# Optimization experiments

Hardware: AMD Instinct MI355X
Metric: run time of the kernel (lower is better)

The kernel has to match this reference:

```python
import jax, jax.numpy as jnp
import numpy as np

F_DIM = 4096
HID = 256
COR = 32
N_FRAMES = 200
NB = 30
TS = 9  # 4 + 5 time_steps


def _gru(xg, hg, wx, wh, bx, bh):
    # torch.nn.GRU cell math, gates ordered (r, z, n)
    gx = xg @ wx + bx
    gh = hg @ wh + bh
    xr, xz, xn = jnp.split(gx, 3, axis=-1)
    hr, hz, hn = jnp.split(gh, 3, axis=-1)
    r = jax.nn.sigmoid(xr + hr)
    z = jax.nn.sigmoid(xz + hz)
    n = jnp.tanh(xn + r * hn)
    return (1.0 - z) * n + z * hg


def _sattn(h, mask):
    # parameter-free scaled dot-product attention across active tracks
    d = jnp.asarray(h.shape[-1], h.dtype)
    s = (h @ h.T) / jnp.sqrt(d)
    s = jnp.where(mask[None, :], s, -1e9)
    a = jax.nn.softmax(s, axis=-1)
    out = a @ h
    return jnp.where(mask[:, None], out, h)


def setup_inputs() -> dict:
    key = jax.random.key(0)
    ks = jax.random.split(key, 20)
    flow = jax.random.normal(ks[0], (1, N_FRAMES, NB + 1, F_DIM), jnp.float32)
    x = jax.random.normal(ks[1], (1, N_FRAMES, NB + 1, F_DIM), jnp.float32)
    # y: [track_id, x1,y1,x2,y2, label, conf, d0..d5] -> 13 channels
    track = jnp.broadcast_to(jnp.arange(1, NB + 1, dtype=jnp.float32)[None, None, :, None], (1, N_FRAMES, NB, 1))
    coords = jax.random.uniform(ks[2], (1, N_FRAMES, NB, 4), jnp.float32, 0.0, 1000.0)
    label = jnp.round(jax.random.uniform(ks[3], (1, N_FRAMES, NB, 1), jnp.float32))
    conf = jax.random.uniform(ks[4], (1, N_FRAMES, NB, 1), jnp.float32)
    dist = jax.random.normal(ks[5], (1, N_FRAMES, NB, 6), jnp.float32)
    y = jnp.concatenate([track, coords, label, conf, dist], axis=-1)
    toa = jnp.ones((1, 1), jnp.float32)
    s = 0.02
    p = lambda k, shp: s * jax.random.normal(k, shp, jnp.float32)
    return {
        "x": x, "y": y, "toa": toa, "flow": flow,
        "W_rgb": p(ks[6], (F_DIM, HID)), "b_rgb": jnp.zeros((HID,), jnp.float32),
        "W_bb": p(ks[7], (5, HID)), "b_bb": jnp.zeros((HID,), jnp.float32),
        "W_dd": p(ks[8], (6, HID)), "b_dd": jnp.zeros((HID,), jnp.float32),
        "W_proj": p(ks[9], (HID, COR)), "b_proj": jnp.zeros((COR,), jnp.float32),
        "Wx_c": p(ks[10], (COR, 3 * COR)), "Wh_c": p(ks[11], (COR, 3 * COR)),
        "bx_c": jnp.zeros((3 * COR,), jnp.float32), "bh_c": jnp.zeros((3 * COR,), jnp.float32),
        "Wx_g": p(ks[12], (2 * HID, 3 * HID)), "Wh_g": p(ks[13], (HID, 3 * HID)),
        "bx_g": jnp.zeros((3 * HID,), jnp.float32), "bh_g": jnp.zeros((3 * HID,), jnp.float32),
        "W_out": p(ks[14], (2 * HID + COR, 1)), "b_out": jnp.zeros((1,), jnp.float32),
        "W_pbox": p(ks[15], (2 * HID + COR, 4 * TS)), "b_pbox": jnp.zeros((4 * TS,), jnp.float32),
    }


def reference(x, y, toa, flow, W_rgb, b_rgb, W_bb, b_bb, W_dd, b_dd, W_proj, b_proj,
              Wx_c, Wh_c, bx_c, bh_c, Wx_g, Wh_g, bx_g, bh_g, W_out, b_out, W_pbox, b_pbox):
    T = x.shape[1] - TS
    norm = jnp.array([1920.0, 1200.0, 1920.0, 1200.0], y.dtype)
    nb = y[0, :, :, 1:5] / norm                      # (N, 30, 4) normalized boxes
    # future targets: 9 future frames of normalized boxes, flattened -> (T, 30, 36)
    fut = jnp.concatenate([nb[1 + i:1 + i + T] for i in range(TS)], axis=-1)
    flow_f = flow[0, :T]                             # (T, 31, F)
    yf = y[0, :T]                                    # (T, 30, 13)
    nbf = nb[:T]
    act = yf[..., 0] != 0                            # (T, 30) active-track mask

    def step(carry, inp):
        h, hc, bacc, oacc = carry
        ft, yt, nbt, futt, at = inp
        atf = at.astype(h.dtype)
        rgb = jax.nn.relu(ft @ W_rgb + b_rgb)        # (31, H)
        img = jnp.broadcast_to(rgb[0], (NB, rgb.shape[-1]))
        comb = jnp.concatenate([rgb[1:], img], axis=-1)            # (30, 2H)
        bfeat = jax.nn.relu(jnp.concatenate([nbt, yt[:, 6:7]], axis=-1) @ W_bb + b_bb)
        dfeat = jax.nn.relu(yt[:, 7:13] @ W_dd + b_dd)
        xc = dfeat @ W_proj + b_proj
        hc_n = _gru(xc, hc, Wx_c, Wh_c, bx_c, bh_c)  # CorGRU, output_cor = hidden
        h_n = _gru(comb, h, Wx_g, Wh_g, bx_g, bh_g)
        feat = jnp.concatenate([h_n, bfeat, hc_n], axis=-1)        # (30, 2H+32)
        logit = (feat @ W_out + b_out)[:, 0]
        pbox = feat @ W_pbox + b_pbox                # (30, 36)
        d = pbox - futt
        ad = jnp.abs(d)
        sl1 = jnp.mean(jnp.where(ad < 1.0, 0.5 * d * d, ad - 0.5), axis=-1)  # SmoothL1 per box
        bacc = bacc + jnp.sum(sl1 * atf)
        tgt = yt[:, 5]
        bce = jnp.maximum(logit, 0.0) - logit * tgt + jnp.log1p(jnp.exp(-jnp.abs(logit)))
        oacc = oacc + 0.05 * jnp.sum(bce * atf)
        h2 = jnp.where(at[:, None], h_n, h)
        hc2 = jnp.where(at[:, None], hc_n, hc)
        return (_sattn(h2, at), _sattn(hc2, at), bacc, oacc), None

    init = (jnp.zeros((NB, HID), flow.dtype), jnp.zeros((NB, COR), flow.dtype),
            jnp.zeros((), flow.dtype), jnp.zeros((), flow.dtype))
    (h, hc, bbox_l, obj_l), _ = jax.lax.scan(step, init, (flow_f, yf, nbf, fut, act))
    total = obj_l + bbox_l + 0.3 * bbox_l            # object + bbox + inter(0.3*bbox)
    return total
```

## Files before the change

kernel.cpp:

```cpp
#include <hip/hip_runtime.h>
#include <math.h>
#include <stdint.h>

#define T_STEPS 191
#define NB1 31
#define YS 13
#define NBLK 8

typedef short bf8 __attribute__((ext_vector_type(8)));
typedef float f16x __attribute__((ext_vector_type(16)));

#define MFMA32 __builtin_amdgcn_mfma_f32_32x32x16_bf16

__device__ __forceinline__ float sigmoid_(float x) { return 1.f / (1.f + expf(-x)); }

__device__ __forceinline__ unsigned bf16b(float x){
  unsigned u = __float_as_uint(x);
  return (u + 0x7fffu + ((u>>16)&1u)) >> 16;
}
__device__ __forceinline__ float bf16f(unsigned b){ return __uint_as_float(b<<16); }

__device__ __forceinline__ bf8 ldfrag(const unsigned short* p, int slot){
  uint4 u = *reinterpret_cast<const uint4*>(p + slot*8);
  return __builtin_bit_cast(bf8, u);
}
__device__ __forceinline__ bf8 ldg4(const unsigned* p){
  uint4 u = *reinterpret_cast<const uint4*>(p);
  return __builtin_bit_cast(bf8, u);
}
__device__ __forceinline__ bf8 gather8(const unsigned short* fr, int base){
  unsigned w0 = (unsigned)fr[base]    | ((unsigned)fr[base+8]<<16);
  unsigned w1 = (unsigned)fr[base+16] | ((unsigned)fr[base+24]<<16);
  unsigned w2 = (unsigned)fr[base+32] | ((unsigned)fr[base+40]<<16);
  unsigned w3 = (unsigned)fr[base+48] | ((unsigned)fr[base+56]<<16);
  uint4 u; u.x=w0; u.y=w1; u.z=w2; u.w=w3;
  return __builtin_bit_cast(bf8, u);
}
__device__ __forceinline__ f16x zf16(){
  f16x v;
#pragma unroll
  for (int q=0;q<16;++q) v[q]=0.f;
  return v;
}
__device__ __forceinline__ int aslot(int m, int k){
  return ((k>>4)*64 + m + ((k>>3)&1)*32)*8 + (k&7);
}

__device__ __forceinline__ void store_dw_mall_f(float* p, float v) {
    asm volatile("global_store_dword %0, %1, off sc0 sc1"
                 :: "v"((uintptr_t)p), "v"(v) : "memory");
}
__device__ __forceinline__ void store_dw_mall_u(unsigned* p, unsigned v) {
    asm volatile("global_store_dword %0, %1, off sc0 sc1"
                 :: "v"((uintptr_t)p), "v"(v) : "memory");
}
__device__ __forceinline__ void atomic_inc_mall(unsigned* p) {
    asm volatile("global_atomic_add %0, %1, off sc1"
                 :: "v"((uintptr_t)p), "v"(1u) : "memory");
}
__device__ __forceinline__ unsigned load_u32_mall(const unsigned* p) {
    unsigned v;
    asm volatile("global_load_dword %0, %1, off sc0 sc1\n\ts_waitcnt vmcnt(0)"
                 : "=v"(v) : "v"((uintptr_t)p) : "memory");
    return v;
}

template <bool GATHER, bool RELU>
__global__ __launch_bounds__(256) void gemm_tiled(
    const float* __restrict__ A, const float* __restrict__ B,
    const float* __restrict__ bias, float* __restrict__ C,
    int M, int N, int K)
{
    __shared__ float As[16][65];
    __shared__ float Bs[16][65];
    const int tid = threadIdx.x;
    const int tm = tid >> 4, tn = tid & 15;
    const int rowBase = blockIdx.y * 64;
    const int colBase = blockIdx.x * 64;
    float acc[4][4] = {};
    for (int kt = 0; kt < K; kt += 16) {
        #pragma unroll
        for (int l = 0; l < 4; ++l) {
            const int idx = tid + l * 256;
            const int kk = idx & 15, rr = idx >> 4;
            const int row = rowBase + rr;
            float v = 0.f;
            if (row < M) {
                if (GATHER) {
                    const int t = row / 30, i = row - t * 30;
                    const int k = kt + kk;
                    const int src = (k < 256) ? ((t * NB1 + i + 1) * 256 + k)
                                              : (t * NB1 * 256 + (k - 256));
                    v = A[src];
                } else {
                    v = A[(size_t)row * K + kt + kk];
                }
            }
            As[kk][rr] = v;
            const int nn = idx & 63, k2 = idx >> 6;
            Bs[k2][nn] = B[(size_t)(kt + k2) * N + colBase + nn];
        }
        __syncthreads();
        #pragma unroll
        for (int kk = 0; kk < 16; ++kk) {
            float a[4], b[4];
            #pragma unroll
            for (int i = 0; i < 4; ++i) a[i] = As[kk][tm * 4 + i];
            #pragma unroll
            for (int j = 0; j < 4; ++j) b[j] = Bs[kk][tn * 4 + j];
            #pragma unroll
            for (int i = 0; i < 4; ++i)
                #pragma unroll
                for (int j = 0; j < 4; ++j)
                    acc[i][j] = fmaf(a[i], b[j], acc[i][j]);
        }
        __syncthreads();
    }
    #pragma unroll
    for (int i = 0; i < 4; ++i) {
        const int row = rowBase + tm * 4 + i;
        if (row < M) {
            #pragma unroll
            for (int j = 0; j < 4; ++j) {
                const int col = colBase + tn * 4 + j;
                float v = acc[i][j] + bias[col];
                if (RELU) v = fmaxf(v, 0.f);
                C[(size_t)row * N + col] = v;
            }
        }
    }
}

__global__ __launch_bounds__(256) void prep_wg(const float* __restrict__ Whg,
                                               unsigned* __restrict__ wpg)
{
    const int idx = blockIdx.x * 256 + threadIdx.x;
    const int j  = idx & 3;
    const int l  = (idx >> 2) & 63;
    const int kb = (idx >> 8) & 15;
    const int nt = idx >> 12;
    const int g = nt / 3, gate = nt - g * 3;
    const int col = gate * 256 + g * 32 + (l & 31);
    const int k2 = kb * 8 + ((l >> 5) << 2) + j;
    const unsigned lo = bf16b(Whg[(size_t)(2 * k2) * 768 + col]);
    const unsigned hi = bf16b(Whg[(size_t)(2 * k2 + 1) * 768 + col]);
    wpg[idx] = lo | (hi << 16);
}

__global__ __launch_bounds__(256) void prep_hd(const float* __restrict__ Wpbox,
                                               const float* __restrict__ Wout,
                                               unsigned* __restrict__ hdh,
                                               unsigned* __restrict__ hdl)
{
    const int idx = blockIdx.x * 256 + threadIdx.x;
    if (idx >= 9216) return;
    const int j = idx & 3;
    const int l = (idx >> 2) & 63;
    const int kbnt = idx >> 8;
    const int kb = kbnt % 18, nt = kbnt / 18;
    const int d = nt * 32 + (l & 31);
    const int k0 = kb * 16 + ((l >> 5) << 3) + 2 * j;
    float v0 = 0.f, v1 = 0.f;
    if (d < 37) {
        const int r0 = (k0 < 256) ? k0 : 512 + (k0 - 256);
        const int r1 = (k0 + 1 < 256) ? (k0 + 1) : 512 + (k0 + 1 - 256);
        v0 = (d < 36) ? Wpbox[(size_t)r0 * 36 + d] : Wout[r0];
        v1 = (d < 36) ? Wpbox[(size_t)r1 * 36 + d] : Wout[r1];
    }
    const unsigned h0 = bf16b(v0), h1 = bf16b(v1);
    const unsigned l0 = bf16b(v0 - bf16f(h0)), l1 = bf16b(v1 - bf16f(h1));
    hdh[idx] = h0 | (h1 << 16);
    hdl[idx] = l0 | (l1 << 16);
}

__global__ __launch_bounds__(256) void prep_hcw(const float* __restrict__ Whc,
                                                unsigned* __restrict__ hch,
                                                unsigned* __restrict__ hcl)
{
    const int idx = blockIdx.x * 256 + threadIdx.x;
    if (idx >= 1536) return;
    const int j = idx & 3;
    const int l = (idx >> 2) & 63;
    const int kb = (idx >> 8) & 1;
    const int nt = idx >> 9;
    const int col = nt * 32 + (l & 31);
    const int k0 = kb * 16 + ((l >> 5) << 3) + 2 * j;
    const float v0 = Whc[k0 * 96 + col];
    const float v1 = Whc[(k0 + 1) * 96 + col];
    const unsigned h0 = bf16b(v0), h1 = bf16b(v1);
    const unsigned l0 = bf16b(v0 - bf16f(h0)), l1 = bf16b(v1 - bf16f(h1));
    hch[idx] = h0 | (h1 << 16);
    hcl[idx] = l0 | (l1 << 16);
}

__global__ void prep_bias(const float* __restrict__ bxg, const float* __restrict__ bhg,
                          const float* __restrict__ bxc, const float* __restrict__ bhc,
                          float* __restrict__ biasg, float* __restrict__ biasc)
{
    const int t = threadIdx.x;
    if (t < 768) biasg[t] = bxg[t] + (t < 512 ? bhg[t] : 0.f);
    if (t < 96)  biasc[t] = bxc[t] + (t < 64 ? bhc[t] : 0.f);
}

__global__ __launch_bounds__(256) void precomp_kernel(
    const float* __restrict__ y,
    const float* __restrict__ Wbb, const float* __restrict__ bbb,
    const float* __restrict__ Wdd, const float* __restrict__ bdd,
    const float* __restrict__ Wproj, const float* __restrict__ bproj,
    const float* __restrict__ Wxc, const float* __restrict__ biasc,
    const float* __restrict__ Wpbox, const float* __restrict__ bpbox,
    const float* __restrict__ Wout, const float* __restrict__ bout,
    float* __restrict__ gxc, float* __restrict__ pbox_b, float* __restrict__ logit_b)
{
    const int m = blockIdx.x;
    const int tid = threadIdx.x;
    __shared__ float bf[256], df[256], xcs[32], yl[16];
    if (tid < YS) yl[tid] = y[m * YS + tid];
    __syncthreads();
    const float invnorm[4] = {1.f/1920.f, 1.f/1200.f, 1.f/1920.f, 1.f/1200.f};
    {
        float s = bbb[tid];
        s = fmaf(yl[1] * invnorm[0], Wbb[0 * 256 + tid], s);
        s = fmaf(yl[2] * invnorm[1], Wbb[1 * 256 + tid], s);
        s = fmaf(yl[3] * invnorm[2], Wbb[2 * 256 + tid], s);
        s = fmaf(yl[4] * invnorm[3], Wbb[3 * 256 + tid], s);
        s = fmaf(yl[6],              Wbb[4 * 256 + tid], s);
        bf[tid] = fmaxf(s, 0.f);
    }
    {
        float s = bdd[tid];
        #pragma unroll
        for (int k = 0; k < 6; ++k) s = fmaf(yl[7 + k], Wdd[k * 256 + tid], s);
        df[tid] = fmaxf(s, 0.f);
    }
    __syncthreads();
    {
        const int c = tid >> 3, p = tid & 7;
        float s = 0.f;
        for (int k = p; k < 256; k += 8) s = fmaf(df[k], Wproj[k * 32 + c], s);
        s += __shfl_xor(s, 1); s += __shfl_xor(s, 2); s += __shfl_xor(s, 4);
        if (p == 0) xcs[c] = s + bproj[c];
    }
    __syncthreads();
    if (tid < 96) {
        float s = biasc[tid];
        #pragma unroll
        for (int k = 0; k < 32; ++k) s = fmaf(xcs[k], Wxc[k * 96 + tid], s);
        gxc[m * 96 + tid] = s;
    }
    {
        const int d = tid >> 2, p = tid & 3;
        if (d < 37) {
            float s = 0.f;
            if (d < 36) {
                for (int k = p; k < 256; k += 4) s = fmaf(bf[k], Wpbox[(256 + k) * 36 + d], s);
            } else {
                for (int k = p; k < 256; k += 4) s = fmaf(bf[k], Wout[256 + k], s);
            }
            s += __shfl_xor(s, 1); s += __shfl_xor(s, 2);
            if (p == 0) {
                if (d < 36) pbox_b[m * 36 + d] = s + bpbox[d];
                else        logit_b[m] = s + bout[0];
            }
        }
    }
}

__global__ __launch_bounds__(512, 2) void seq8(
    const float* __restrict__ y,
    const float* __restrict__ gxg,
    const float* __restrict__ gxc,
    const float* __restrict__ pbox_b,
    const float* __restrict__ logit_b,
    const unsigned* __restrict__ wpg,
    const unsigned* __restrict__ hdh, const unsigned* __restrict__ hdl,
    const unsigned* __restrict__ hch, const unsigned* __restrict__ hcl,
    const float* __restrict__ bhg,
    const float* __restrict__ bhc,
    unsigned* __restrict__ h2x,
    float* __restrict__ pbx,
    unsigned* __restrict__ bar,
    float* __restrict__ parts)
{
    const int tid = threadIdx.x;
    const int bb = blockIdx.x;
    const int lane = tid & 63, wid = tid >> 6;
    const int half = lane >> 5, ln31 = lane & 31;

    __shared__ __align__(16) unsigned wgl[12288];
    __shared__ __align__(16) unsigned short hA_hi[8192], hA_lo[8192];
    __shared__ __align__(16) unsigned short hnf_hi[1024], hnf_lo[1024];
    __shared__ __align__(16) unsigned short cf_hi[1024],  cf_lo[1024];
    __shared__ __align__(16) unsigned short cnf_hi[1024], cnf_lo[1024];
    __shared__ __align__(16) unsigned short wf_hi[1024],  wf_lo[1024];
    __shared__ __align__(16) unsigned short cwf_hi[1024], cwf_lo[1024];
    __shared__ float exch[6144];
    __shared__ float gxgs[2880];
    __shared__ float gxcs[2880];
    __shared__ float hcst[1056];
    __shared__ float actf[32], bhnl[32], bhcl[32], red[16];

    {
        const unsigned* wsrc = wpg + (size_t)(3 * bb) * 4096;
        for (int i = tid; i < 12288; i += 512) wgl[i] = wsrc[i];
    }
    for (int i = tid; i < 8192; i += 512){ hA_hi[i] = 0; hA_lo[i] = 0; }
    for (int i = tid; i < 1024; i += 512){
        hnf_hi[i]=0; hnf_lo[i]=0; cf_hi[i]=0; cf_lo[i]=0;
        cnf_hi[i]=0; cnf_lo[i]=0; wf_hi[i]=0; wf_lo[i]=0;
        cwf_hi[i]=0; cwf_lo[i]=0;
    }
    for (int i = tid; i < 1056; i += 512) hcst[i] = 0.f;
    if (tid < 32){ bhnl[tid] = bhg[512 + bb*32 + tid]; bhcl[tid] = bhc[64 + tid]; }
    float bacc = 0.f, oacc = 0.f;
    __syncthreads();

    for (int t = 0; t < T_STEPS; ++t) {
        const int m0 = t * 30;
        const int dbuf = t & 1;
        unsigned* h2b = h2x + dbuf * 8192;
        float* pbb = pbx + dbuf * 9600;

        float4 sg0, sg1, sc0v, sc1v;
        const bool hasg = (tid < 360);
        if (hasg){
            { const int i = tid;       const int obj = i/24, r24 = i - obj*24;
              sg0 = *(const float4*)(gxg + (size_t)(m0+obj)*768 + (r24>>3)*256 + bb*32 + (r24&7)*4); }
            { const int i = tid + 360; const int obj = i/24, r24 = i - obj*24;
              sg1 = *(const float4*)(gxg + (size_t)(m0+obj)*768 + (r24>>3)*256 + bb*32 + (r24&7)*4); }
        }
        const bool hasc = (bb == 7) && (tid < 360);
        if (hasc){
            { const int i = tid;       const int obj = i/24, c4 = i - obj*24;
              sc0v = *(const float4*)(gxc + (size_t)(m0+obj)*96 + c4*4); }
            { const int i = tid + 360; const int obj = i/24, c4 = i - obj*24;
              sc1v = *(const float4*)(gxc + (size_t)(m0+obj)*96 + c4*4); }
        }
        if (tid < 32) actf[tid] = (tid < 30 && y[(size_t)(m0+tid)*YS] != 0.f) ? 1.f : 0.f;

        if (wid < 3){
            f16x acc = zf16();
            const unsigned* wb = wgl + wid * 4096;
#pragma unroll 4
            for (int kb = 0; kb < 16; ++kb){
                const bf8 bw = ldg4(wb + (kb*64 + lane)*4);
                const bf8 ah = ldfrag(hA_hi, kb*64 + lane);
                const bf8 al = ldfrag(hA_lo, kb*64 + lane);
                acc = MFMA32(ah, bw, acc, 0,0,0);
                acc = MFMA32(al, bw, acc, 0,0,0);
            }
#pragma unroll
            for (int q = 0; q < 16; ++q){
                const int row = (q&3) + ((q>>2)<<3) + (half<<2);
                exch[wid*1024 + row*32 + ln31] = acc[q];
            }
        } else if (wid < 6 && bb == 7){
            const int g3 = wid - 3;
            f16x acc = zf16();
#pragma unroll
            for (int kb = 0; kb < 2; ++kb){
                const bf8 ah = ldfrag(cf_hi, kb*64 + lane);
                const bf8 al = ldfrag(cf_lo, kb*64 + lane);
                const bf8 wh = ldg4(hch + ((g3*2 + kb)*64 + lane)*4);
                const bf8 wl = ldg4(hcl + ((g3*2 + kb)*64 + lane)*4);
                acc = MFMA32(ah, wh, acc, 0,0,0);
                acc = MFMA32(ah, wl, acc, 0,0,0);
                acc = MFMA32(al, wh, acc, 0,0,0);
            }
#pragma unroll
            for (int q = 0; q < 16; ++q){
                const int row = (q&3) + ((q>>2)<<3) + (half<<2);
                exch[(3+g3)*1024 + row*32 + ln31] = acc[q];
            }
        }
        if (hasg){
            { const int i = tid;       const int obj = i/24, r24 = i - obj*24;
              *(float4*)(gxgs + obj*96 + r24*4) = sg0; }
            { const int i = tid + 360; const int obj = i/24, r24 = i - obj*24;
              *(float4*)(gxgs + obj*96 + r24*4) = sg1; }
        }
        if (hasc){
            { const int i = tid;       const int obj = i/24, c4 = i - obj*24;
              *(float4*)(gxcs + obj*96 + c4*4) = sc0v; }
            { const int i = tid + 360; const int obj = i/24, c4 = i - obj*24;
              *(float4*)(gxcs + obj*96 + c4*4) = sc1v; }
        }
        __syncthreads();

        if (tid < 480){
#pragma unroll
            for (int s = 0; s < 2; ++s){
                const int e = tid*2 + s;
                const int obj = e >> 5, dim = e & 31;
                const float rv = sigmoid_(exch[obj*32 + dim]        + gxgs[obj*96 + dim]);
                const float zv = sigmoid_(exch[1024 + obj*32 + dim] + gxgs[obj*96 + 32 + dim]);
                const float nv = tanhf(gxgs[obj*96 + 64 + dim]
                                       + rv*(exch[2048 + obj*32 + dim] + bhnl[dim]));
                const int sl = aslot(obj, bb*32 + dim);
                const float h = bf16f(hA_hi[sl]) + bf16f(hA_lo[sl]);
                const float hnv = (1.f - zv)*nv + zv*h;
                const float h2 = (actf[obj] > 0.f) ? hnv : h;
                const unsigned hb = bf16b(h2), lb = bf16b(h2 - bf16f(hb));
                store_dw_mall_u(h2b + sl, hb | (lb << 16));
                const int sl2 = aslot(obj, dim);
                const unsigned nh = bf16b(hnv), nl = bf16b(hnv - bf16f(nh));
                hnf_hi[sl2] = (unsigned short)nh; hnf_lo[sl2] = (unsigned short)nl;
            }
            if (bb == 7){
#pragma unroll
                for (int s = 0; s < 2; ++s){
                    const int e = tid*2 + s;
                    const int obj = e >> 5, cd = e & 31;
                    const float rv = sigmoid_(exch[3072 + obj*32 + cd] + gxcs[obj*96 + cd]);
                    const float zv = sigmoid_(exch[4096 + obj*32 + cd] + gxcs[obj*96 + 32 + cd]);
                    const float nv = tanhf(gxcs[obj*96 + 64 + cd]
                                           + rv*(exch[5120 + obj*32 + cd] + bhcl[cd]));
                    const float hc = hcst[obj*33 + cd];
                    const float cnv = (1.f - zv)*nv + zv*hc;
                    const float c2 = (actf[obj] > 0.f) ? cnv : hc;
                    hcst[obj*33 + cd] = c2;
                    const int sl2 = aslot(obj, cd);
                    const unsigned hb = bf16b(c2), lb = bf16b(c2 - bf16f(hb));
                    cf_hi[sl2] = (unsigned short)hb; cf_lo[sl2] = (unsigned short)lb;
                    const unsigned nh = bf16b(cnv), nl = bf16b(cnv - bf16f(nh));
                    cnf_hi[sl2] = (unsigned short)nh; cnf_lo[sl2] = (unsigned short)nl;
                }
            }
        }
        __syncthreads();

        if (wid < 2){
            f16x hp = zf16();
#pragma unroll
            for (int kb = 0; kb < 2; ++kb){
                const bf8 ah = ldfrag(hnf_hi, kb*64 + lane);
                const bf8 al = ldfrag(hnf_lo, kb*64 + lane);
                const int kbg = 2*bb + kb;
                const bf8 wh = ldg4(hdh + ((wid*18 + kbg)*64 + lane)*4);
                const bf8 wl = ldg4(hdl + ((wid*18 + kbg)*64 + lane)*4);
                hp = MFMA32(ah, wh, hp, 0,0,0);
                hp = MFMA32(al, wh, hp, 0,0,0);
                hp = MFMA32(ah, wl, hp, 0,0,0);
            }
            if (bb == 7){
#pragma unroll
                for (int kb = 0; kb < 2; ++kb){
                    const bf8 ah = ldfrag(cnf_hi, kb*64 + lane);
                    const bf8 al = ldfrag(cnf_lo, kb*64 + lane);
                    const bf8 wh = ldg4(hdh + ((wid*18 + 16 + kb)*64 + lane)*4);
                    const bf8 wl = ldg4(hdl + ((wid*18 + 16 + kb)*64 + lane)*4);
                    hp = MFMA32(ah, wh, hp, 0,0,0);
                    hp = MFMA32(al, wh, hp, 0,0,0);
                    hp = MFMA32(ah, wl, hp, 0,0,0);
                }
            }
            const int d = wid*32 + ln31;
            if (d < 37){
#pragma unroll
                for (int q = 0; q < 16; ++q){
                    const int obj = (q&3) + ((q>>2)<<3) + (half<<2);
                    if (obj < 30) store_dw_mall_f(pbb + (obj*40 + d)*8 + bb, hp[q]);
                }
            }
        }

        asm volatile("s_waitcnt vmcnt(0)" ::: "memory");
        __syncthreads();
        if (tid == 0){
            atomic_inc_mall(bar);
            const unsigned tgtc = (unsigned)(NBLK * (t + 1));
            unsigned cur;
            do { asm volatile("s_sleep 1" :::); cur = load_u32_mall(bar); } while (cur < tgtc);
        }
        __syncthreads();

        {
            const int nOb = (bb == 7) ? 2 : 4;
            if (tid < nOb * 37){
                const int oo = tid / 37, d = tid - oo*37;
                const int obj = bb*4 + oo;
                if (actf[obj] > 0.f){
                    const float* pp = pbb + (obj*40 + d)*8;
                    float4 f0, f1;
                    asm volatile("global_load_dwordx4 %0, %2, off sc0 sc1\n\t"
                                 "global_load_dwordx4 %1, %3, off sc0 sc1\n\t"
                                 "s_waitcnt vmcnt(0)"
                                 : "=v"(f0), "=v"(f1)
                                 : "v"((uintptr_t)pp), "v"((uintptr_t)(pp+4)) : "memory");
                    const float sum8 = f0.x+f0.y+f0.z+f0.w + f1.x+f1.y+f1.z+f1.w;
                    const int m = m0 + obj;
                    if (d < 36){
                        const int s4 = d >> 2, cc = d & 3;
                        const float fn = (cc & 1) ? (1.f/1200.f) : (1.f/1920.f);
                        const float fu = y[(size_t)((t+1+s4)*30 + obj)*YS + 1 + cc] * fn;
                        const float df = sum8 + pbox_b[(size_t)m*36 + d] - fu;
                        const float ad = fabsf(df);
                        bacc += ((ad < 1.f) ? 0.5f*df*df : ad - 0.5f) * (1.f/36.f);
                    } else {
                        const float l = sum8 + logit_b[m];
                        const float tg = y[(size_t)m*YS + 5];
                        oacc += 0.05f * (fmaxf(l, 0.f) - l*tg + log1pf(expf(-fabsf(l))));
                    }
                }
            }
        }
        {
            unsigned uu[16];
#pragma unroll
            for (int j = 0; j < 16; ++j){
                const unsigned* sp = h2b + tid + j*512;
                asm volatile("global_load_dword %0, %1, off sc0 sc1"
                             : "=v"(uu[j]) : "v"((uintptr_t)sp) : "memory");
            }
            asm volatile("s_waitcnt vmcnt(0)" ::: "memory");
#pragma unroll
            for (int j = 0; j < 16; ++j){
                const int idx = tid + j*512;
                hA_hi[idx] = (unsigned short)(uu[j] & 0xffffu);
                hA_lo[idx] = (unsigned short)(uu[j] >> 16);
            }
        }
        __syncthreads();

        if (wid < 3){
            f16x s = zf16();
#pragma unroll 4
            for (int kb = 0; kb < 16; ++kb){
                const bf8 ah = ldfrag(hA_hi, kb*64 + lane);
                const bf8 al = ldfrag(hA_lo, kb*64 + lane);
                if (wid == 0)      s = MFMA32(ah, ah, s, 0,0,0);
                else if (wid == 1) s = MFMA32(ah, al, s, 0,0,0);
                else               s = MFMA32(al, ah, s, 0,0,0);
            }
#pragma unroll
            for (int q = 0; q < 16; ++q){
                const int row = (q&3) + ((q>>2)<<3) + (half<<2);
                exch[wid*1024 + row*32 + ln31] = s[q];
            }
        } else if (wid == 3 && bb == 7){
            f16x s = zf16();
#pragma unroll
            for (int kb = 0; kb < 2; ++kb){
                const bf8 ah = ldfrag(cf_hi, kb*64 + lane);
                const bf8 al = ldfrag(cf_lo, kb*64 + lane);
                s = MFMA32(ah, ah, s, 0,0,0);
                s = MFMA32(ah, al, s, 0,0,0);
                s = MFMA32(al, ah, s, 0,0,0);
            }
#pragma unroll
            for (int q = 0; q < 16; ++q){
                const int row = (q&3) + ((q>>2)<<3) + (half<<2);
                exch[3072 + row*32 + ln31] = s[q];
            }
        }
        __syncthreads();

        if (wid == 0 && lane < 30){
            float sv[30]; float mx = -1e30f;
#pragma unroll
            for (int j = 0; j < 30; ++j){
                float x = exch[lane*32 + j] + exch[1024 + lane*32 + j] + exch[2048 + lane*32 + j];
                x = (actf[j] > 0.f) ? x * 0.0625f : -1e9f;
                sv[j] = x; mx = fmaxf(mx, x);
            }
            float sum = 0.f;
#pragma unroll
            for (int j = 0; j < 30; ++j){ sv[j] = expf(sv[j] - mx); sum += sv[j]; }
            const float inv = 1.f / sum;
#pragma unroll
            for (int j = 0; j < 32; ++j){
                const float w = (j < 30) ? sv[j]*inv : 0.f;
                const unsigned hb = bf16b(w), lb = bf16b(w - bf16f(hb));
                const int sl = aslot(lane, j);
                wf_hi[sl] = (unsigned short)hb; wf_lo[sl] = (unsigned short)lb;
            }
        } else if (wid == 1 && bb == 7 && lane < 30){
            float sv[30]; float mx = -1e30f;
#pragma unroll
            for (int j = 0; j < 30; ++j){
                float x = exch[3072 + lane*32 + j];
                x = (actf[j] > 0.f) ? x * 0.17677669529663687f : -1e9f;
                sv[j] = x; mx = fmaxf(mx, x);
            }
            float sum = 0.f;
#pragma unroll
            for (int j = 0; j < 30; ++j){ sv[j] = expf(sv[j] - mx); sum += sv[j]; }
            const float inv = 1.f / sum;
#pragma unroll
            for (int j = 0; j < 32; ++j){
                const float w = (j < 30) ? sv[j]*inv : 0.f;
                const unsigned hb = bf16b(w), lb = bf16b(w - bf16f(hb));
                const int sl = aslot(lane, j);
                cwf_hi[sl] = (unsigned short)hb; cwf_lo[sl] = (unsigned short)lb;
            }
        }
        __syncthreads();

        {
            const int dd = wid*32 + ln31;
            f16x ao = zf16();
#pragma unroll
            for (int kb2 = 0; kb2 < 2; ++kb2){
                const bf8 wh = ldfrag(wf_hi, kb2*64 + lane);
                const bf8 wl = ldfrag(wf_lo, kb2*64 + lane);
                const int base = ((dd>>4)*64 + kb2*16 + (half<<3) + ((dd>>3)&1)*32)*8 + (dd&7);
                const bf8 bh = gather8(hA_hi, base);
                const bf8 bl = gather8(hA_lo, base);
                ao = MFMA32(wh, bh, ao, 0,0,0);
                ao = MFMA32(wh, bl, ao, 0,0,0);
                ao = MFMA32(wl, bh, ao, 0,0,0);
            }
#pragma unroll
            for (int q = 0; q < 16; ++q){
                const int obj = (q&3) + ((q>>2)<<3) + (half<<2);
                const int sl = aslot(obj, dd);
                const float h2v = bf16f(hA_hi[sl]) + bf16f(hA_lo[sl]);
                const float v = (actf[obj] > 0.f) ? ao[q] : h2v;
                const unsigned hb = bf16b(v), lb = bf16b(v - bf16f(hb));
                hA_hi[sl] = (unsigned short)hb; hA_lo[sl] = (unsigned short)lb;
            }
        }
        if (bb == 7 && wid == 0){
            f16x co = zf16();
#pragma unroll
            for (int kb2 = 0; kb2 < 2; ++kb2){
                const bf8 wh = ldfrag(cwf_hi, kb2*64 + lane);
                const bf8 wl = ldfrag(cwf_lo, kb2*64 + lane);
                const int base = ((ln31>>4)*64 + kb2*16 + (half<<3) + ((ln31>>3)&1)*32)*8 + (ln31&7);
                const bf8 bh = gather8(cf_hi, base);
                const bf8 bl = gather8(cf_lo, base);
                co = MFMA32(wh, bh, co, 0,0,0);
                co = MFMA32(wh, bl, co, 0,0,0);
                co = MFMA32(wl, bh, co, 0,0,0);
            }
#pragma unroll
            for (int q = 0; q < 16; ++q){
                const int obj = (q&3) + ((q>>2)<<3) + (half<<2);
                const float c2v = hcst[obj*33 + ln31];
                const float v = (actf[obj] > 0.f) ? co[q] : c2v;
                hcst[obj*33 + ln31] = v;
                const int sl = aslot(obj, ln31);
                const unsigned hb = bf16b(v), lb = bf16b(v - bf16f(hb));
                cf_hi[sl] = (unsigned short)hb; cf_lo[sl] = (unsigned short)lb;
            }
        }
        __syncthreads();
    }

#pragma unroll
    for (int o = 1; o < 64; o <<= 1){ bacc += __shfl_xor(bacc, o); oacc += __shfl_xor(oacc, o); }
    if (lane == 0){ red[wid] = bacc; red[8 + wid] = oacc; }
    __syncthreads();
    if (tid == 0){
        float b = 0.f, o = 0.f;
        for (int i = 0; i < 8; ++i){ b += red[i]; o += red[8 + i]; }
        parts[bb] = b; parts[8 + bb] = o;
    }
}

__global__ void reduce_kernel(const float* __restrict__ parts, float* __restrict__ out) {
    if (threadIdx.x == 0) {
        float b = 0.f, o = 0.f;
        for (int i = 0; i < NBLK; ++i) { b += parts[i]; o += parts[8 + i]; }
        out[0] = o + 1.3f * b;
    }
}

extern "C" void kernel_launch(void* const* d_in, const int* in_sizes, int n_in,
                              void* d_out, int out_size, void* d_ws, size_t ws_size,
                              hipStream_t stream) {
    (void)in_sizes; (void)n_in; (void)out_size; (void)ws_size;
    const float* y      = (const float*)d_in[1];
    const float* flow   = (const float*)d_in[3];
    const float* W_rgb  = (const float*)d_in[4];
    const float* b_rgb  = (const float*)d_in[5];
    const float* W_bb   = (const float*)d_in[6];
    const float* b_bb   = (const float*)d_in[7];
    const float* W_dd   = (const float*)d_in[8];
    const float* b_dd   = (const float*)d_in[9];
    const float* W_proj = (const float*)d_in[10];
    const float* b_proj = (const float*)d_in[11];
    const float* Wx_c   = (const float*)d_in[12];
    const float* Wh_c   = (const float*)d_in[13];
    const float* bx_c   = (const float*)d_in[14];
    const float* bh_c   = (const float*)d_in[15];
    const float* Wx_g   = (const float*)d_in[16];
    const float* Wh_g   = (const float*)d_in[17];
    const float* bx_g   = (const float*)d_in[18];
    const float* bh_g   = (const float*)d_in[19];
    const float* W_out  = (const float*)d_in[20];
    const float* b_out  = (const float*)d_in[21];
    const float* W_pbox = (const float*)d_in[22];
    const float* b_pbox = (const float*)d_in[23];
    float* out = (float*)d_out;

    char* ws = (char*)d_ws;
    unsigned* bar = (unsigned*)ws;
    unsigned* h2x = (unsigned*)(ws + 256);
    float* pbx    = (float*)(ws + 256 + 65536);
    float* parts  = (float*)(ws + 256 + 65536 + 76800);
    float* base   = (float*)(ws + 256 + 65536 + 76800 + 64);
    size_t off = 0;
    float* rgb    = base + off; off += (size_t)5921 * 256;
    float* gxg    = base + off; off += (size_t)5730 * 768;
    float* gxc    = base + off; off += (size_t)5730 * 96;
    float* pboxb  = base + off; off += (size_t)5730 * 36;
    float* logitb = base + off; off += 5760;
    float* biasg  = base + off; off += 768;
    float* biasc  = base + off; off += 96;
    unsigned* wpg = (unsigned*)(base + off); off += 98304;
    unsigned* hdh = (unsigned*)(base + off); off += 9216;
    unsigned* hdl = (unsigned*)(base + off); off += 9216;
    unsigned* hch = (unsigned*)(base + off); off += 1536;
    unsigned* hcl = (unsigned*)(base + off); off += 1536;

    (void)hipMemsetAsync(d_ws, 0, 256 + 65536, stream);

    prep_bias<<<1, 768, 0, stream>>>(bx_g, bh_g, bx_c, bh_c, biasg, biasc);
    prep_wg<<<384, 256, 0, stream>>>(Wh_g, wpg);
    prep_hd<<<36, 256, 0, stream>>>(W_pbox, W_out, hdh, hdl);
    prep_hcw<<<6, 256, 0, stream>>>(Wh_c, hch, hcl);

    gemm_tiled<false, true><<<dim3(4, 93), 256, 0, stream>>>(flow, W_rgb, b_rgb, rgb, 5921, 256, 4096);
    gemm_tiled<true, false><<<dim3(12, 90), 256, 0, stream>>>(rgb, Wx_g, biasg, gxg, 5730, 768, 512);
    precomp_kernel<<<5730, 256, 0, stream>>>(y, W_bb, b_bb, W_dd, b_dd, W_proj, b_proj,
                                             Wx_c, biasc, W_pbox, b_pbox, W_out, b_out,
                                             gxc, pboxb, logitb);
    seq8<<<NBLK, 512, 0, stream>>>(y, gxg, gxc, pboxb, logitb, wpg, hdh, hdl, hch, hcl,
                                   bh_g, bh_c, h2x, pbx, bar, parts);
    reduce_kernel<<<1, 64, 0, stream>>>(parts, out);
}
```

Baseline: 4.662 ms.

## Replicate CorGRU and head projection per block to drop cross-block pbox exchange

Each of the 8 persistent blocks now computes the small CorGRU and the full pbox/logit head projection locally from its gathered copy of the hidden state, instead of block 7 doing CorGRU alone and blocks exchanging partial head sums through global memory. The per-step hidden-state exchange is rewritten to use wider vectorized stores and loads, and the 65KB pbx scratch buffer and its memset are removed. This cuts global traffic and work on the serialized per-step critical path, at the cost of redundant MFMA work in every block and a lower occupancy hint.

Result: faster. 4.140 ms (-11.2%).

```diff
diff --git a/kernel.cpp b/kernel.cpp
--- a/kernel.cpp
+++ b/kernel.cpp
@@ -46,12 +46,9 @@
   return ((k>>4)*64 + m + ((k>>3)&1)*32)*8 + (k&7);
 }
 
-__device__ __forceinline__ void store_dw_mall_f(float* p, float v) {
-    asm volatile("global_store_dword %0, %1, off sc0 sc1"
-                 :: "v"((uintptr_t)p), "v"(v) : "memory");
-}
-__device__ __forceinline__ void store_dw_mall_u(unsigned* p, unsigned v) {
-    asm volatile("global_store_dword %0, %1, off sc0 sc1"
+__device__ __forceinline__ void store_dwx2_mall(unsigned* p, unsigned a, unsigned b){
+    const unsigned long long v = ((unsigned long long)b << 32) | (unsigned long long)a;
+    asm volatile("global_store_dwordx2 %0, %1, off sc0 sc1"
                  :: "v"((uintptr_t)p), "v"(v) : "memory");
 }
 __device__ __forceinline__ void atomic_inc_mall(unsigned* p) {
@@ -266,7 +263,7 @@
     }
 }
 
-__global__ __launch_bounds__(512, 2) void seq8(
+__global__ __launch_bounds__(512, 1) void seqx(
     const float* __restrict__ y,
     const float* __restrict__ gxg,
     const float* __restrict__ gxc,
@@ -278,7 +275,6 @@
     const float* __restrict__ bhg,
     const float* __restrict__ bhc,
     unsigned* __restrict__ h2x,
-    float* __restrict__ pbx,
     unsigned* __restrict__ bar,
     float* __restrict__ parts)
 {
@@ -289,15 +285,14 @@
 
     __shared__ __align__(16) unsigned wgl[12288];
     __shared__ __align__(16) unsigned short hA_hi[8192], hA_lo[8192];
-    __shared__ __align__(16) unsigned short hnf_hi[1024], hnf_lo[1024];
     __shared__ __align__(16) unsigned short cf_hi[1024],  cf_lo[1024];
-    __shared__ __align__(16) unsigned short cnf_hi[1024], cnf_lo[1024];
     __shared__ __align__(16) unsigned short wf_hi[1024],  wf_lo[1024];
     __shared__ __align__(16) unsigned short cwf_hi[1024], cwf_lo[1024];
     __shared__ float exch[6144];
     __shared__ float gxgs[2880];
     __shared__ float gxcs[2880];
     __shared__ float hcst[1056];
+    __shared__ float pbl[1280];
     __shared__ float actf[32], bhnl[32], bhcl[32], red[16];
 
     {
@@ -306,37 +301,31 @@
     }
     for (int i = tid; i < 8192; i += 512){ hA_hi[i] = 0; hA_lo[i] = 0; }
     for (int i = tid; i < 1024; i += 512){
-        hnf_hi[i]=0; hnf_lo[i]=0; cf_hi[i]=0; cf_lo[i]=0;
-        cnf_hi[i]=0; cnf_lo[i]=0; wf_hi[i]=0; wf_lo[i]=0;
-        cwf_hi[i]=0; cwf_lo[i]=0;
+        cf_hi[i]=0; cf_lo[i]=0; wf_hi[i]=0; wf_lo[i]=0; cwf_hi[i]=0; cwf_lo[i]=0;
     }
     for (int i = tid; i < 1056; i += 512) hcst[i] = 0.f;
     if (tid < 32){ bhnl[tid] = bhg[512 + bb*32 + tid]; bhcl[tid] = bhc[64 + tid]; }
     float bacc = 0.f, oacc = 0.f;
     __syncthreads();
 
-    for (int t = 0; t < T_STEPS; ++t) {
+    for (int t = 0; t < T_STEPS; ++t){
         const int m0 = t * 30;
         const int dbuf = t & 1;
         unsigned* h2b = h2x + dbuf * 8192;
-        float* pbb = pbx + dbuf * 9600;
-
+
+        if (tid < 32) actf[tid] = (tid < 30 && y[(size_t)(m0 + tid) * YS] != 0.f) ? 1.f : 0.f;
         float4 sg0, sg1, sc0v, sc1v;
         const bool hasg = (tid < 360);
         if (hasg){
-            { const int i = tid;       const int obj = i/24, r24 = i - obj*24;
-              sg0 = *(const float4*)(gxg + (size_t)(m0+obj)*768 + (r24>>3)*256 + bb*32 + (r24&7)*4); }
-            { const int i = tid + 360; const int obj = i/24, r24 = i - obj*24;
-              sg1 = *(const float4*)(gxg + (size_t)(m0+obj)*768 + (r24>>3)*256 + bb*32 + (r24&7)*4); }
-        }
-        const bool hasc = (bb == 7) && (tid < 360);
-        if (hasc){
-            { const int i = tid;       const int obj = i/24, c4 = i - obj*24;
-              sc0v = *(const float4*)(gxc + (size_t)(m0+obj)*96 + c4*4); }
-            { const int i = tid + 360; const int obj = i/24, c4 = i - obj*24;
-              sc1v = *(const float4*)(gxc + (size_t)(m0+obj)*96 + c4*4); }
-        }
-        if (tid < 32) actf[tid] = (tid < 30 && y[(size_t)(m0+tid)*YS] != 0.f) ? 1.f : 0.f;
+            { const int i = tid;       const int obj = i/12, r12 = i - obj*12;
+              sg0 = *(const float4*)(gxg + (size_t)(m0+obj)*768 + (r12>>2)*256 + bb*32 + (r12&3)*8); }
+            { const int i = tid;       const int obj = i/12, r12 = i - obj*12;
+              sg1 = *(const float4*)(gxg + (size_t)(m0+obj)*768 + (r12>>2)*256 + bb*32 + (r12&3)*8 + 4); }
+            { const int i = tid;       const int obj = i/12, c12 = i - obj*12;
+              sc0v = *(const float4*)(gxc + (size_t)(m0+obj)*96 + c12*8); }
+            { const int i = tid;       const int obj = i/12, c12 = i - obj*12;
+              sc1v = *(const float4*)(gxc + (size_t)(m0+obj)*96 + c12*8 + 4); }
+        }
 
         if (wid < 3){
             f16x acc = zf16();
@@ -354,36 +343,31 @@
                 const int row = (q&3) + ((q>>2)<<3) + (half<<2);
                 exch[wid*1024 + row*32 + ln31] = acc[q];
             }
-        } else if (wid < 6 && bb == 7){
+        } else if (wid < 6){
             const int g3 = wid - 3;
-            f16x acc = zf16();
+            f16x cacc = zf16();
 #pragma unroll
             for (int kb = 0; kb < 2; ++kb){
                 const bf8 ah = ldfrag(cf_hi, kb*64 + lane);
                 const bf8 al = ldfrag(cf_lo, kb*64 + lane);
                 const bf8 wh = ldg4(hch + ((g3*2 + kb)*64 + lane)*4);
                 const bf8 wl = ldg4(hcl + ((g3*2 + kb)*64 + lane)*4);
-                acc = MFMA32(ah, wh, acc, 0,0,0);
-                acc = MFMA32(ah, wl, acc, 0,0,0);
-                acc = MFMA32(al, wh, acc, 0,0,0);
+                cacc = MFMA32(ah, wh, cacc, 0,0,0);
+                cacc = MFMA32(ah, wl, cacc, 0,0,0);
+                cacc = MFMA32(al, wh, cacc, 0,0,0);
             }
 #pragma unroll
             for (int q = 0; q < 16; ++q){
                 const int row = (q&3) + ((q>>2)<<3) + (half<<2);
-                exch[(3+g3)*1024 + row*32 + ln31] = acc[q];
+                exch[(3+g3)*1024 + row*32 + ln31] = cacc[q];
             }
         }
         if (hasg){
-            { const int i = tid;       const int obj = i/24, r24 = i - obj*24;
-              *(float4*)(gxgs + obj*96 + r24*4) = sg0; }
-            { const int i = tid + 360; const int obj = i/24, r24 = i - obj*24;
-              *(float4*)(gxgs + obj*96 + r24*4) = sg1; }
-        }
-        if (hasc){
-            { const int i = tid;       const int obj = i/24, c4 = i - obj*24;
-              *(float4*)(gxcs + obj*96 + c4*4) = sc0v; }
-            { const int i = tid + 360; const int obj = i/24, c4 = i - obj*24;
-              *(float4*)(gxcs + obj*96 + c4*4) = sc1v; }
+            const int obj = tid/12, r12 = tid - obj*12;
+            *(float4*)(gxgs + obj*96 + r12*8)     = sg0;
+            *(float4*)(gxgs + obj*96 + r12*8 + 4) = sg1;
+            *(float4*)(gxcs + obj*96 + r12*8)     = sc0v;
+            *(float4*)(gxcs + obj*96 + r12*8 + 4) = sc1v;
         }
         __syncthreads();
 
@@ -401,71 +385,38 @@
                 const float hnv = (1.f - zv)*nv + zv*h;
                 const float h2 = (actf[obj] > 0.f) ? hnv : h;
                 const unsigned hb = bf16b(h2), lb = bf16b(h2 - bf16f(hb));
-                store_dw_mall_u(h2b + sl, hb | (lb << 16));
-                const int sl2 = aslot(obj, dim);
-                const unsigned nh = bf16b(hnv), nl = bf16b(hnv - bf16f(nh));
-                hnf_hi[sl2] = (unsigned short)nh; hnf_lo[sl2] = (unsigned short)nl;
-            }
-            if (bb == 7){
-#pragma unroll
-                for (int s = 0; s < 2; ++s){
-                    const int e = tid*2 + s;
-                    const int obj = e >> 5, cd = e & 31;
-                    const float rv = sigmoid_(exch[3072 + obj*32 + cd] + gxcs[obj*96 + cd]);
-                    const float zv = sigmoid_(exch[4096 + obj*32 + cd] + gxcs[obj*96 + 32 + cd]);
-                    const float nv = tanhf(gxcs[obj*96 + 64 + cd]
-                                           + rv*(exch[5120 + obj*32 + cd] + bhcl[cd]));
-                    const float hc = hcst[obj*33 + cd];
-                    const float cnv = (1.f - zv)*nv + zv*hc;
-                    const float c2 = (actf[obj] > 0.f) ? cnv : hc;
-                    hcst[obj*33 + cd] = c2;
-                    const int sl2 = aslot(obj, cd);
-                    const unsigned hb = bf16b(c2), lb = bf16b(c2 - bf16f(hb));
-                    cf_hi[sl2] = (unsigned short)hb; cf_lo[sl2] = (unsigned short)lb;
-                    const unsigned nh = bf16b(cnv), nl = bf16b(cnv - bf16f(nh));
-                    cnf_hi[sl2] = (unsigned short)nh; cnf_lo[sl2] = (unsigned short)nl;
-                }
-            }
-        }
-        __syncthreads();
-
-        if (wid < 2){
-            f16x hp = zf16();
-#pragma unroll
-            for (int kb = 0; kb < 2; ++kb){
-                const bf8 ah = ldfrag(hnf_hi, kb*64 + lane);
-                const bf8 al = ldfrag(hnf_lo, kb*64 + lane);
-                const int kbg = 2*bb + kb;
-                const bf8 wh = ldg4(hdh + ((wid*18 + kbg)*64 + lane)*4);
-                const bf8 wl = ldg4(hdl + ((wid*18 + kbg)*64 + lane)*4);
-                hp = MFMA32(ah, wh, hp, 0,0,0);
-                hp = MFMA32(al, wh, hp, 0,0,0);
-                hp = MFMA32(ah, wl, hp, 0,0,0);
-            }
-            if (bb == 7){
-#pragma unroll
-                for (int kb = 0; kb < 2; ++kb){
-                    const bf8 ah = ldfrag(cnf_hi, kb*64 + lane);
-                    const bf8 al = ldfrag(cnf_lo, kb*64 + lane);
-                    const bf8 wh = ldg4(hdh + ((wid*18 + 16 + kb)*64 + lane)*4);
-                    const bf8 wl = ldg4(hdl + ((wid*18 + 16 + kb)*64 + lane)*4);
-                    hp = MFMA32(ah, wh, hp, 0,0,0);
-                    hp = MFMA32(al, wh, hp, 0,0,0);
-                    hp = MFMA32(ah, wl, hp, 0,0,0);
-                }
-            }
-            const int d = wid*32 + ln31;
-            if (d < 37){
-#pragma unroll
-                for (int q = 0; q < 16; ++q){
-                    const int obj = (q&3) + ((q>>2)<<3) + (half<<2);
-                    if (obj < 30) store_dw_mall_f(pbb + (obj*40 + d)*8 + bb, hp[q]);
-                }
-            }
-        }
-
+                hA_hi[sl] = (unsigned short)hb; hA_lo[sl] = (unsigned short)lb;
+            }
+        }
+        __syncthreads();
+
+        {
+            const int s0 = 1024*bb + tid*2;
+            const unsigned d0 = (unsigned)hA_hi[s0]   | ((unsigned)hA_lo[s0]   << 16);
+            const unsigned d1 = (unsigned)hA_hi[s0+1] | ((unsigned)hA_lo[s0+1] << 16);
+            store_dwx2_mall(h2b + s0, d0, d1);
+        }
+        if (tid < 480){
+#pragma unroll
+            for (int s = 0; s < 2; ++s){
+                const int e = tid*2 + s;
+                const int obj = e >> 5, cd = e & 31;
+                const float rv = sigmoid_(exch[3072 + obj*32 + cd] + gxcs[obj*96 + cd]);
+                const float zv = sigmoid_(exch[4096 + obj*32 + cd] + gxcs[obj*96 + 32 + cd]);
+                const float nv = tanhf(gxcs[obj*96 + 64 + cd]
+                                       + rv*(exch[5120 + obj*32 + cd] + bhcl[cd]));
+                const float hc = hcst[obj*33 + cd];
+                const float cnv = (1.f - zv)*nv + zv*hc;
+                const float c2 = (actf[obj] > 0.f) ? cnv : hc;
+                hcst[obj*33 + cd] = c2;
+                const int sl = aslot(obj, cd);
+                const unsigned hb = bf16b(c2), lb = bf16b(c2 - bf16f(hb));
+                cf_hi[sl] = (unsigned short)hb; cf_lo[sl] = (unsigned short)lb;
+            }
+        }
         asm volatile("s_waitcnt vmcnt(0)" ::: "memory");
         __syncthreads();
+
         if (tid == 0){
             atomic_inc_mall(bar);
             const unsigned tgtc = (unsigned)(NBLK * (t + 1));
@@ -475,49 +426,26 @@
         __syncthreads();
 
         {
-            const int nOb = (bb == 7) ? 2 : 4;
-            if (tid < nOb * 37){
-                const int oo = tid / 37, d = tid - oo*37;
-                const int obj = bb*4 + oo;
-                if (actf[obj] > 0.f){
-                    const float* pp = pbb + (obj*40 + d)*8;
-                    float4 f0, f1;
-                    asm volatile("global_load_dwordx4 %0, %2, off sc0 sc1\n\t"
-                                 "global_load_dwordx4 %1, %3, off sc0 sc1\n\t"
-                                 "s_waitcnt vmcnt(0)"
-                                 : "=v"(f0), "=v"(f1)
-                                 : "v"((uintptr_t)pp), "v"((uintptr_t)(pp+4)) : "memory");
-                    const float sum8 = f0.x+f0.y+f0.z+f0.w + f1.x+f1.y+f1.z+f1.w;
-                    const int m = m0 + obj;
-                    if (d < 36){
-                        const int s4 = d >> 2, cc = d & 3;
-                        const float fn = (cc & 1) ? (1.f/1200.f) : (1.f/1920.f);
-                        const float fu = y[(size_t)((t+1+s4)*30 + obj)*YS + 1 + cc] * fn;
-                        const float df = sum8 + pbox_b[(size_t)m*36 + d] - fu;
-                        const float ad = fabsf(df);
-                        bacc += ((ad < 1.f) ? 0.5f*df*df : ad - 0.5f) * (1.f/36.f);
-                    } else {
-                        const float l = sum8 + logit_b[m];
-                        const float tg = y[(size_t)m*YS + 5];
-                        oacc += 0.05f * (fmaxf(l, 0.f) - l*tg + log1pf(expf(-fabsf(l))));
-                    }
+            uint4 v0, v1, v2, v3;
+            const unsigned* p0 = h2b + 0*2048 + tid*4;
+            const unsigned* p1 = h2b + 1*2048 + tid*4;
+            const unsigned* p2 = h2b + 2*2048 + tid*4;
+            const unsigned* p3 = h2b + 3*2048 + tid*4;
+            asm volatile("global_load_dwordx4 %0, %1, off sc0 sc1" : "=v"(v0) : "v"((uintptr_t)p0) : "memory");
+            asm volatile("global_load_dwordx4 %0, %1, off sc0 sc1" : "=v"(v1) : "v"((uintptr_t)p1) : "memory");
+            asm volatile("global_load_dwordx4 %0, %1, off sc0 sc1" : "=v"(v2) : "v"((uintptr_t)p2) : "memory");
+            asm volatile("global_load_dwordx4 %0, %1, off sc0 sc1" : "=v"(v3) : "v"((uintptr_t)p3) : "memory");
+            asm volatile("s_waitcnt vmcnt(0)" ::: "memory");
+            const uint4 vv[4] = {v0, v1, v2, v3};
+#pragma unroll
+            for (int j = 0; j < 4; ++j){
+                const int sl = j*2048 + tid*4;
+                const unsigned dw[4] = {vv[j].x, vv[j].y, vv[j].z, vv[j].w};
+#pragma unroll
+                for (int k = 0; k < 4; ++k){
+                    hA_hi[sl+k] = (unsigned short)(dw[k] & 0xffffu);
+                    hA_lo[sl+k] = (unsigned short)(dw[k] >> 16);
                 }
-            }
-        }
-        {
-            unsigned uu[16];
-#pragma unroll
-            for (int j = 0; j < 16; ++j){
-                const unsigned* sp = h2b + tid + j*512;
-                asm volatile("global_load_dword %0, %1, off sc0 sc1"
-                             : "=v"(uu[j]) : "v"((uintptr_t)sp) : "memory");
-            }
-            asm volatile("s_waitcnt vmcnt(0)" ::: "memory");
-#pragma unroll
-            for (int j = 0; j < 16; ++j){
-                const int idx = tid + j*512;
-                hA_hi[idx] = (unsigned short)(uu[j] & 0xffffu);
-                hA_lo[idx] = (unsigned short)(uu[j] >> 16);
             }
         }
         __syncthreads();
@@ -537,7 +465,38 @@
                 const int row = (q&3) + ((q>>2)<<3) + (half<<2);
                 exch[wid*1024 + row*32 + ln31] = s[q];
             }
-        } else if (wid == 3 && bb == 7){
+        } else if (wid < 5){
+            const int nt = wid - 3;
+            f16x h1 = zf16(), h2v = zf16(), h3 = zf16();
+#pragma unroll 4
+            for (int kb = 0; kb < 16; ++kb){
+                const bf8 ah = ldfrag(hA_hi, kb*64 + lane);
+                const bf8 al = ldfrag(hA_lo, kb*64 + lane);
+                const bf8 wh = ldg4(hdh + ((nt*18 + kb)*64 + lane)*4);
+                const bf8 wl = ldg4(hdl + ((nt*18 + kb)*64 + lane)*4);
+                h1 = MFMA32(ah, wh, h1, 0,0,0);
+                h2v = MFMA32(al, wh, h2v, 0,0,0);
+                h3 = MFMA32(ah, wl, h3, 0,0,0);
+            }
+#pragma unroll
+            for (int kb = 16; kb < 18; ++kb){
+                const bf8 ah = ldfrag(cf_hi, (kb-16)*64 + lane);
+                const bf8 al = ldfrag(cf_lo, (kb-16)*64 + lane);
+                const bf8 wh = ldg4(hdh + ((nt*18 + kb)*64 + lane)*4);
+                const bf8 wl = ldg4(hdl + ((nt*18 + kb)*64 + lane)*4);
+                h1 = MFMA32(ah, wh, h1, 0,0,0);
+                h2v = MFMA32(al, wh, h2v, 0,0,0);
+                h3 = MFMA32(ah, wl, h3, 0,0,0);
+            }
+            const int d = nt*32 + ln31;
+            if (d < 37){
+#pragma unroll
+                for (int q = 0; q < 16; ++q){
+                    const int obj = (q&3) + ((q>>2)<<3) + (half<<2);
+                    if (obj < 30) pbl[obj*40 + d] = h1[q] + h2v[q] + h3[q];
+                }
+            }
+        } else if (wid == 5){
             f16x s = zf16();
 #pragma unroll
             for (int kb = 0; kb < 2; ++kb){
@@ -555,43 +514,69 @@
         }
         __syncthreads();
 
-        if (wid == 0 && lane < 30){
-            float sv[30]; float mx = -1e30f;
-#pragma unroll
-            for (int j = 0; j < 30; ++j){
-                float x = exch[lane*32 + j] + exch[1024 + lane*32 + j] + exch[2048 + lane*32 + j];
-                x = (actf[j] > 0.f) ? x * 0.0625f : -1e9f;
-                sv[j] = x; mx = fmaxf(mx, x);
-            }
-            float sum = 0.f;
-#pragma unroll
-            for (int j = 0; j < 30; ++j){ sv[j] = expf(sv[j] - mx); sum += sv[j]; }
-            const float inv = 1.f / sum;
-#pragma unroll
-            for (int j = 0; j < 32; ++j){
-                const float w = (j < 30) ? sv[j]*inv : 0.f;
-                const unsigned hb = bf16b(w), lb = bf16b(w - bf16f(hb));
-                const int sl = aslot(lane, j);
-                wf_hi[sl] = (unsigned short)hb; wf_lo[sl] = (unsigned short)lb;
-            }
-        } else if (wid == 1 && bb == 7 && lane < 30){
-            float sv[30]; float mx = -1e30f;
-#pragma unroll
-            for (int j = 0; j < 30; ++j){
-                float x = exch[3072 + lane*32 + j];
-                x = (actf[j] > 0.f) ? x * 0.17677669529663687f : -1e9f;
-                sv[j] = x; mx = fmaxf(mx, x);
-            }
-            float sum = 0.f;
-#pragma unroll
-            for (int j = 0; j < 30; ++j){ sv[j] = expf(sv[j] - mx); sum += sv[j]; }
-            const float inv = 1.f / sum;
-#pragma unroll
-            for (int j = 0; j < 32; ++j){
-                const float w = (j < 30) ? sv[j]*inv : 0.f;
-                const unsigned hb = bf16b(w), lb = bf16b(w - bf16f(hb));
-                const int sl = aslot(lane, j);
-                cwf_hi[sl] = (unsigned short)hb; cwf_lo[sl] = (unsigned short)lb;
+        if (wid == 0){
+            if (lane < 30){
+                float sv[30]; float mx = -1e30f;
+#pragma unroll
+                for (int j = 0; j < 30; ++j){
+                    float x = exch[lane*32 + j] + exch[1024 + lane*32 + j] + exch[2048 + lane*32 + j];
+                    x = (actf[j] > 0.f) ? x * 0.0625f : -1e9f;
+                    sv[j] = x; mx = fmaxf(mx, x);
+                }
+                float sum = 0.f;
+#pragma unroll
+                for (int j = 0; j < 30; ++j){ sv[j] = expf(sv[j] - mx); sum += sv[j]; }
+                const float inv = 1.f / sum;
+#pragma unroll
+                for (int j = 0; j < 32; ++j){
+                    const float w = (j < 30) ? sv[j]*inv : 0.f;
+                    const unsigned hb = bf16b(w), lb = bf16b(w - bf16f(hb));
+                    const int sl = aslot(lane, j);
+                    wf_hi[sl] = (unsigned short)hb; wf_lo[sl] = (unsigned short)lb;
+                }
+            }
+        } else if (wid == 1){
+            if (lane < 30){
+                float sv[30]; float mx = -1e30f;
+#pragma unroll
+                for (int j = 0; j < 30; ++j){
+                    float x = exch[3072 + lane*32 + j];
+                    x = (actf[j] > 0.f) ? x * 0.17677669529663687f : -1e9f;
+                    sv[j] = x; mx = fmaxf(mx, x);
+                }
+                float sum = 0.f;
+#pragma unroll
+                for (int j = 0; j < 30; ++j){ sv[j] = expf(sv[j] - mx); sum += sv[j]; }
+                const float inv = 1.f / sum;
+#pragma unroll
+                for (int j = 0; j < 32; ++j){
+                    const float w = (j < 30) ? sv[j]*inv : 0.f;
+                    const unsigned hb = bf16b(w), lb = bf16b(w - bf16f(hb));
+                    const int sl = aslot(lane, j);
+                    cwf_hi[sl] = (unsigned short)hb; cwf_lo[sl] = (unsigned short)lb;
+                }
+            }
+        } else {
+            const int nObj = (bb == 7) ? 2 : 4;
+            const int c = tid - 128;
+            if (c < nObj * 37){
+                const int oo = c / 37, d = c - oo*37;
+                const int obj = bb*4 + oo;
+                if (actf[obj] > 0.f){
+                    const int m = m0 + obj;
+                    if (d < 36){
+                        const int s4 = d >> 2, cc = d & 3;
+                        const float fn = (cc & 1) ? (1.f/1200.f) : (1.f/1920.f);
+                        const float fu = y[(size_t)((t + 1 + s4)*30 + obj)*YS + 1 + cc] * fn;
+                        const float df = pbl[obj*40 + d] + pbox_b[(size_t)m*36 + d] - fu;
+                        const float ad = fabsf(df);
+                        bacc += ((ad < 1.f) ? 0.5f*df*df : ad - 0.5f) * (1.f/36.f);
+                    } else {
+                        const float l = pbl[obj*40 + 36] + logit_b[m];
+                        const float tg = y[(size_t)m*YS + 5];
+                        oacc += 0.05f * (fmaxf(l, 0.f) - l*tg + log1pf(expf(-fabsf(l))));
+                    }
+                }
             }
         }
         __syncthreads();
@@ -620,7 +605,7 @@
                 hA_hi[sl] = (unsigned short)hb; hA_lo[sl] = (unsigned short)lb;
             }
         }
-        if (bb == 7 && wid == 0){
+        if (wid == 7){
             f16x co = zf16();
 #pragma unroll
             for (int kb2 = 0; kb2 < 2; ++kb2){
@@ -636,8 +621,7 @@
 #pragma unroll
             for (int q = 0; q < 16; ++q){
                 const int obj = (q&3) + ((q>>2)<<3) + (half<<2);
-                const float c2v = hcst[obj*33 + ln31];
-                const float v = (actf[obj] > 0.f) ? co[q] : c2v;
+                const float v = (actf[obj] > 0.f) ? co[q] : hcst[obj*33 + ln31];
                 hcst[obj*33 + ln31] = v;
                 const int sl = aslot(obj, ln31);
                 const unsigned hb = bf16b(v), lb = bf16b(v - bf16f(hb));
@@ -697,9 +681,8 @@
     char* ws = (char*)d_ws;
     unsigned* bar = (unsigned*)ws;
     unsigned* h2x = (unsigned*)(ws + 256);
-    float* pbx    = (float*)(ws + 256 + 65536);
-    float* parts  = (float*)(ws + 256 + 65536 + 76800);
-    float* base   = (float*)(ws + 256 + 65536 + 76800 + 64);
+    float* parts  = (float*)(ws + 256 + 65536);
+    float* base   = (float*)(ws + 256 + 65536 + 64);
     size_t off = 0;
     float* rgb    = base + off; off += (size_t)5921 * 256;
     float* gxg    = base + off; off += (size_t)5730 * 768;
@@ -714,7 +697,7 @@
     unsigned* hch = (unsigned*)(base + off); off += 1536;
     unsigned* hcl = (unsigned*)(base + off); off += 1536;
 
-    (void)hipMemsetAsync(d_ws, 0, 256 + 65536, stream);
+    (void)hipMemsetAsync(d_ws, 0, 256, stream);
 
     prep_bias<<<1, 768, 0, stream>>>(bx_g, bh_g, bx_c, bh_c, biasg, biasc);
     prep_wg<<<384, 256, 0, stream>>>(Wh_g, wpg);
@@ -726,7 +709,7 @@
     precomp_kernel<<<5730, 256, 0, stream>>>(y, W_bb, b_bb, W_dd, b_dd, W_proj, b_proj,
                                              Wx_c, biasc, W_pbox, b_pbox, W_out, b_out,
                                              gxc, pboxb, logitb);
-    seq8<<<NBLK, 512, 0, stream>>>(y, gxg, gxc, pboxb, logitb, wpg, hdh, hdl, hch, hcl,
-                                   bh_g, bh_c, h2x, pbx, bar, parts);
+    seqx<<<NBLK, 512, 0, stream>>>(y, gxg, gxc, pboxb, logitb, wpg, hdh, hdl, hch, hcl,
+                                   bh_g, bh_c, h2x, bar, parts);
     reduce_kernel<<<1, 64, 0, stream>>>(parts, out);
 }
```
